# Optimization experiments

Hardware: AMD Instinct MI355X
Metric: run time of the kernel (lower is better)

## Reference

```python
import jax, jax.numpy as jnp
import numpy as np

B, N, D, C, E, K = 8, 8192, 128, 128, 8, 2


def setup_inputs() -> dict:
    key = jax.random.key(0)
    k0, k1, k2 = jax.random.split(key, 3)
    x = jax.random.normal(k0, (B, N, D), dtype=jnp.float32)
    router_w = jax.random.normal(k1, (D, E), dtype=jnp.float32) * 0.05
    router_b = jnp.zeros((E,), dtype=jnp.float32)
    expert_w = jax.random.normal(k2, (E, D, C), dtype=jnp.float32) * (1.0 / np.sqrt(D))
    expert_b = jnp.zeros((E, C), dtype=jnp.float32)
    return {"x": x, "router_w": router_w, "router_b": router_b,
            "expert_w": expert_w, "expert_b": expert_b}


def reference(x, router_w, router_b, expert_w, expert_b):
    # Router: softmax over experts, then top-k gating with renormalization.
    router_probs = jax.nn.softmax(x @ router_w + router_b, axis=-1)      # [B,N,E]
    top_p, top_i = jax.lax.top_k(router_probs, K)                        # [B,N,K]
    top_p = top_p / jnp.sum(top_p, axis=-1, keepdims=True)
    # Naive all-expert dense compute (faithful to original): [B,N,E,C]
    expert_out = jnp.einsum('bnd,edc->bnec', x, expert_w) + expert_b
    # Gather the K selected experts per token: [B,N,K,C]
    gathered = jnp.take_along_axis(expert_out, top_i[..., None], axis=2)
    # Weighted combine over selected experts: [B,N,C]
    return jnp.einsum('bnk,bnkc->bnc', top_p, gathered)
```

## Files before the change

kernel.cpp:

```cpp
#include <hip/hip_runtime.h>
#include <hip/hip_bf16.h>
#include <stdint.h>

#define Dd 128
#define Cc 128
#define Ee 8
#define TM 64
#define NTOK 65536

using f32x4  = __attribute__((ext_vector_type(4))) float;
using short8 = __attribute__((ext_vector_type(8))) short;
typedef unsigned short u16;

__device__ inline u16 f2bf(float f) {
    union { __hip_bfloat16 h; u16 u; } cv;
    cv.h = __float2bfloat16(f);
    return cv.u;
}

__global__ __launch_bounds__(256) void transpose_w(const float* __restrict__ w,
                                                   u16* __restrict__ wt) {
    int idx = blockIdx.x * 256 + threadIdx.x;
    int d = idx & 127;
    int c = (idx >> 7) & 127;
    int e = idx >> 14;
    wt[idx] = f2bf(w[(e << 14) + (d << 7) + c]);
}

__global__ __launch_bounds__(256, 3) void moe_main(
    const float* __restrict__ x,
    const float* __restrict__ rw,
    const float* __restrict__ rb,
    const float* __restrict__ eb,
    const u16*   __restrict__ wt,
    float*       __restrict__ out)
{
    __shared__ __align__(16) unsigned char ldsA[Cc * Dd * 2];
    __shared__ __align__(16) u16 Xs[TM * Dd];
    __shared__ float glg[TM * Ee];

    float* Xf = (float*)ldsA;
    u16*   Ws = (u16*)ldsA;

    const int tid = threadIdx.x;
    const int t0  = blockIdx.x * TM;

    {
        const float4* src = (const float4*)(x + (size_t)t0 * Dd);
        float4* dst = (float4*)Xf;
        #pragma unroll
        for (int j = 0; j < 8; ++j) dst[j * 256 + tid] = src[j * 256 + tid];
    }
    __syncthreads();

    #pragma unroll
    for (int i = 0; i < 2; ++i) {
        int p  = tid * 2 + i;
        int tk = p >> 3, e = p & 7;
        double acc = (double)rb[e];
        const float* xr = Xf + tk * Dd;
        for (int d = 0; d < Dd; ++d)
            acc += (double)xr[d] * (double)rw[d * Ee + e];
        glg[p] = (float)acc;
    }

    #pragma unroll
    for (int j = 0; j < 4; ++j) {
        int fc = j * 256 + tid;
        int r = fc >> 4, c = fc & 15;
        const float4* s = (const float4*)(Xf + r * Dd + c * 8);
        float4 a = s[0], b = s[1];
        short8 v;
        v[0] = (short)f2bf(a.x); v[1] = (short)f2bf(a.y);
        v[2] = (short)f2bf(a.z); v[3] = (short)f2bf(a.w);
        v[4] = (short)f2bf(b.x); v[5] = (short)f2bf(b.y);
        v[6] = (short)f2bf(b.z); v[7] = (short)f2bf(b.w);
        *(short8*)&Xs[r * Dd + (((c ^ (r & 7)) & 15) << 3)] = v;
    }
    __syncthreads();

    if (tid < TM) {
        float l[Ee];
        #pragma unroll
        for (int e = 0; e < Ee; ++e) l[e] = glg[tid * Ee + e];
        int e0 = 0;
        #pragma unroll
        for (int e = 1; e < Ee; ++e) if (l[e] > l[e0]) e0 = e;
        int e1 = (e0 == 0) ? 1 : 0;
        #pragma unroll
        for (int e = 0; e < Ee; ++e)
            if (e != e0 && l[e] > l[e1]) e1 = e;
        float g1 = __expf(l[e1] - l[e0]);
        float s  = 1.0f + g1;
        float g0 = 1.0f / s; g1 = g1 / s;
        #pragma unroll
        for (int e = 0; e < Ee; ++e) glg[tid * Ee + e] = 0.0f;
        glg[tid * Ee + e0] = g0;
        glg[tid * Ee + e1] = g1;
    }

    const int lane = tid & 63;
    const int wv   = tid >> 6;
    const int m0   = (wv >> 1) * 32;
    const int n0   = (wv & 1) * 64;
    const int ln15 = lane & 15;
    const int kg   = lane >> 4;

    f32x4 oacc[2][4] = {};

    for (int e = 0; e < Ee; ++e) {
        __syncthreads();
        {
            const u16* src = wt + ((size_t)e << 14);
            #pragma unroll
            for (int j = 0; j < 8; ++j) {
                int fc = j * 256 + tid;
                int r = fc >> 4, c = fc & 15;
                short8 v = *(const short8*)(src + (fc << 3));
                *(short8*)&Ws[r * Dd + (((c ^ (r & 7)) & 15) << 3)] = v;
            }
        }
        __syncthreads();

        f32x4 acc[2][4] = {};
        #pragma unroll
        for (int ks = 0; ks < 4; ++ks) {
            short8 af[2], bfr[4];
            #pragma unroll
            for (int mi = 0; mi < 2; ++mi) {
                int r = m0 + mi * 16 + ln15;
                af[mi] = *(const short8*)
                    &Xs[r * Dd + ((((ks * 4 + kg) ^ (r & 7)) & 15) << 3)];
            }
            #pragma unroll
            for (int ni = 0; ni < 4; ++ni) {
                int r = n0 + ni * 16 + ln15;
                bfr[ni] = *(const short8*)
                    &Ws[r * Dd + ((((ks * 4 + kg) ^ (r & 7)) & 15) << 3)];
            }
            #pragma unroll
            for (int mi = 0; mi < 2; ++mi)
                #pragma unroll
                for (int ni = 0; ni < 4; ++ni)
                    acc[mi][ni] = __builtin_amdgcn_mfma_f32_16x16x32_bf16(
                        af[mi], bfr[ni], acc[mi][ni], 0, 0, 0);
        }

        #pragma unroll
        for (int mi = 0; mi < 2; ++mi) {
            #pragma unroll
            for (int r = 0; r < 4; ++r) {
                float g = glg[(m0 + mi * 16 + kg * 4 + r) * Ee + e];
                #pragma unroll
                for (int ni = 0; ni < 4; ++ni) {
                    float b = eb[e * Cc + n0 + ni * 16 + ln15];
                    oacc[mi][ni][r] += g * (acc[mi][ni][r] + b);
                }
            }
        }
    }

    #pragma unroll
    for (int mi = 0; mi < 2; ++mi)
        #pragma unroll
        for (int r = 0; r < 4; ++r) {
            size_t row = (size_t)(t0 + m0 + mi * 16 + kg * 4 + r);
            #pragma unroll
            for (int ni = 0; ni < 4; ++ni)
                out[row * Cc + n0 + ni * 16 + ln15] = oacc[mi][ni][r];
        }
}

extern "C" void kernel_launch(void* const* d_in, const int* in_sizes, int n_in,
                              void* d_out, int out_size, void* d_ws, size_t ws_size,
                              hipStream_t stream) {
    const float* x  = (const float*)d_in[0];
    const float* rw = (const float*)d_in[1];
    const float* rb = (const float*)d_in[2];
    const float* ew = (const float*)d_in[3];
    const float* eb = (const float*)d_in[4];
    float* out = (float*)d_out;
    u16* wt = (u16*)d_ws;

    transpose_w<<<dim3(512), dim3(256), 0, stream>>>(ew, wt);
    moe_main<<<dim3(NTOK / TM), dim3(256), 0, stream>>>(x, rw, rb, eb, wt, out);
}
```

Measured before the change: 144.3 us.

## Double-buffer expert weights with async LDS loads and keep activations in registers

Expert weights are now written pre-swizzled by the transpose kernel. The main kernel streams each expert's weights into one of two LDS buffers with global_load_lds, so the next expert's tile loads while the current expert's MFMAs run. Activation fragments are loaded straight from global memory into registers as bf16 instead of going through LDS. The router top-2 selection is deferred until after the first expert's matmul. This removes the per-expert load/sync serialization and the X staging, at the cost of more LDS per block (occupancy bound drops from 3 to 2) and a dependence on async-copy completion being ordered before the barriers.

Result: slower. 179.8 us (+24.6%).

```diff
diff --git a/kernel.cpp b/kernel.cpp
--- a/kernel.cpp
+++ b/kernel.cpp
@@ -24,10 +24,28 @@
     int d = idx & 127;
     int c = (idx >> 7) & 127;
     int e = idx >> 14;
-    wt[idx] = f2bf(w[(e << 14) + (d << 7) + c]);
-}
-
-__global__ __launch_bounds__(256, 3) void moe_main(
+    int slot = (d >> 3) ^ (c & 7);
+    wt[(e << 14) + (c << 7) + (slot << 3) + (d & 7)] =
+        f2bf(w[(e << 14) + (d << 7) + c]);
+}
+
+__device__ __forceinline__ void stage_expert(const u16* __restrict__ wt, int e,
+                                             u16* dst, int tid) {
+    const u16* src = wt + ((size_t)e << 14);
+    int wave = tid >> 6;
+    #pragma unroll
+    for (int j = 0; j < 8; ++j) {
+        int chunk = (j << 8) + tid;
+        const u16* g = src + (chunk << 3);
+        u16* l = dst + ((((j << 8) + (wave << 6))) << 3);
+        __builtin_amdgcn_global_load_lds(
+            (const __attribute__((address_space(1))) unsigned int*)g,
+            (__attribute__((address_space(3))) unsigned int*)l,
+            16, 0, 0);
+    }
+}
+
+__global__ __launch_bounds__(256, 2) void moe_main(
     const float* __restrict__ x,
     const float* __restrict__ rw,
     const float* __restrict__ rb,
@@ -35,128 +53,129 @@
     const u16*   __restrict__ wt,
     float*       __restrict__ out)
 {
-    __shared__ __align__(16) unsigned char ldsA[Cc * Dd * 2];
-    __shared__ __align__(16) u16 Xs[TM * Dd];
+    __shared__ __align__(16) u16 Ws[2][Cc * Dd];
     __shared__ float glg[TM * Ee];
 
-    float* Xf = (float*)ldsA;
-    u16*   Ws = (u16*)ldsA;
-
-    const int tid = threadIdx.x;
-    const int t0  = blockIdx.x * TM;
-
-    {
-        const float4* src = (const float4*)(x + (size_t)t0 * Dd);
-        float4* dst = (float4*)Xf;
-        #pragma unroll
-        for (int j = 0; j < 8; ++j) dst[j * 256 + tid] = src[j * 256 + tid];
-    }
-    __syncthreads();
-
-    #pragma unroll
-    for (int i = 0; i < 2; ++i) {
-        int p  = tid * 2 + i;
-        int tk = p >> 3, e = p & 7;
-        double acc = (double)rb[e];
-        const float* xr = Xf + tk * Dd;
-        for (int d = 0; d < Dd; ++d)
-            acc += (double)xr[d] * (double)rw[d * Ee + e];
-        glg[p] = (float)acc;
-    }
-
-    #pragma unroll
-    for (int j = 0; j < 4; ++j) {
-        int fc = j * 256 + tid;
-        int r = fc >> 4, c = fc & 15;
-        const float4* s = (const float4*)(Xf + r * Dd + c * 8);
-        float4 a = s[0], b = s[1];
-        short8 v;
-        v[0] = (short)f2bf(a.x); v[1] = (short)f2bf(a.y);
-        v[2] = (short)f2bf(a.z); v[3] = (short)f2bf(a.w);
-        v[4] = (short)f2bf(b.x); v[5] = (short)f2bf(b.y);
-        v[6] = (short)f2bf(b.z); v[7] = (short)f2bf(b.w);
-        *(short8*)&Xs[r * Dd + (((c ^ (r & 7)) & 15) << 3)] = v;
-    }
-    __syncthreads();
-
-    if (tid < TM) {
-        float l[Ee];
-        #pragma unroll
-        for (int e = 0; e < Ee; ++e) l[e] = glg[tid * Ee + e];
-        int e0 = 0;
-        #pragma unroll
-        for (int e = 1; e < Ee; ++e) if (l[e] > l[e0]) e0 = e;
-        int e1 = (e0 == 0) ? 1 : 0;
-        #pragma unroll
-        for (int e = 0; e < Ee; ++e)
-            if (e != e0 && l[e] > l[e1]) e1 = e;
-        float g1 = __expf(l[e1] - l[e0]);
-        float s  = 1.0f + g1;
-        float g0 = 1.0f / s; g1 = g1 / s;
-        #pragma unroll
-        for (int e = 0; e < Ee; ++e) glg[tid * Ee + e] = 0.0f;
-        glg[tid * Ee + e0] = g0;
-        glg[tid * Ee + e1] = g1;
-    }
-
+    const int tid  = threadIdx.x;
+    const int t0   = blockIdx.x * TM;
     const int lane = tid & 63;
-    const int wv   = tid >> 6;
-    const int m0   = (wv >> 1) * 32;
-    const int n0   = (wv & 1) * 64;
+    const int wave = tid >> 6;
+    const int m0   = (wave >> 1) * 32;
+    const int n0   = (wave & 1) * 64;
     const int ln15 = lane & 15;
     const int kg   = lane >> 4;
 
+    stage_expert(wt, 0, Ws[0], tid);
+
+    {
+        int p  = tid * 2;
+        int tk = p >> 3, e0 = p & 7;
+        const float4* xr = (const float4*)(x + (size_t)(t0 + tk) * Dd);
+        double a0 = (double)rb[e0], a1 = (double)rb[e0 + 1];
+        #pragma unroll 8
+        for (int q = 0; q < 32; ++q) {
+            float4 v = xr[q];
+            #pragma unroll
+            for (int u = 0; u < 4; ++u) {
+                double xv = (double)((const float*)&v)[u];
+                a0 += xv * (double)rw[(q * 4 + u) * Ee + e0];
+                a1 += xv * (double)rw[(q * 4 + u) * Ee + e0 + 1];
+            }
+        }
+        glg[p] = (float)a0;
+        glg[p + 1] = (float)a1;
+    }
+
+    short8 af[2][4];
+    #pragma unroll
+    for (int mi = 0; mi < 2; ++mi) {
+        int r = t0 + m0 + mi * 16 + ln15;
+        #pragma unroll
+        for (int ks = 0; ks < 4; ++ks) {
+            const float4* s = (const float4*)(x + (size_t)r * Dd + (ks * 4 + kg) * 8);
+            float4 a = s[0], b = s[1];
+            short8 v;
+            v[0] = (short)f2bf(a.x); v[1] = (short)f2bf(a.y);
+            v[2] = (short)f2bf(a.z); v[3] = (short)f2bf(a.w);
+            v[4] = (short)f2bf(b.x); v[5] = (short)f2bf(b.y);
+            v[6] = (short)f2bf(b.z); v[7] = (short)f2bf(b.w);
+            af[mi][ks] = v;
+        }
+    }
+
+    __syncthreads();
+
     f32x4 oacc[2][4] = {};
 
     for (int e = 0; e < Ee; ++e) {
-        __syncthreads();
-        {
-            const u16* src = wt + ((size_t)e << 14);
-            #pragma unroll
-            for (int j = 0; j < 8; ++j) {
-                int fc = j * 256 + tid;
-                int r = fc >> 4, c = fc & 15;
-                short8 v = *(const short8*)(src + (fc << 3));
-                *(short8*)&Ws[r * Dd + (((c ^ (r & 7)) & 15) << 3)] = v;
-            }
-        }
-        __syncthreads();
+        const u16* wsc = Ws[e & 1];
+        if (e < Ee - 1) stage_expert(wt, e + 1, Ws[(e + 1) & 1], tid);
 
         f32x4 acc[2][4] = {};
         #pragma unroll
         for (int ks = 0; ks < 4; ++ks) {
-            short8 af[2], bfr[4];
-            #pragma unroll
-            for (int mi = 0; mi < 2; ++mi) {
-                int r = m0 + mi * 16 + ln15;
-                af[mi] = *(const short8*)
-                    &Xs[r * Dd + ((((ks * 4 + kg) ^ (r & 7)) & 15) << 3)];
-            }
+            short8 bfr[4];
+            int cc = ks * 4 + kg;
             #pragma unroll
             for (int ni = 0; ni < 4; ++ni) {
                 int r = n0 + ni * 16 + ln15;
-                bfr[ni] = *(const short8*)
-                    &Ws[r * Dd + ((((ks * 4 + kg) ^ (r & 7)) & 15) << 3)];
+                bfr[ni] = *(const short8*)&wsc[r * Dd + ((cc ^ (r & 7)) << 3)];
             }
             #pragma unroll
             for (int mi = 0; mi < 2; ++mi)
                 #pragma unroll
                 for (int ni = 0; ni < 4; ++ni)
                     acc[mi][ni] = __builtin_amdgcn_mfma_f32_16x16x32_bf16(
-                        af[mi], bfr[ni], acc[mi][ni], 0, 0, 0);
-        }
-
-        #pragma unroll
-        for (int mi = 0; mi < 2; ++mi) {
-            #pragma unroll
-            for (int r = 0; r < 4; ++r) {
-                float g = glg[(m0 + mi * 16 + kg * 4 + r) * Ee + e];
-                #pragma unroll
-                for (int ni = 0; ni < 4; ++ni) {
-                    float b = eb[e * Cc + n0 + ni * 16 + ln15];
-                    oacc[mi][ni][r] += g * (acc[mi][ni][r] + b);
+                        af[mi][ks], bfr[ni], acc[mi][ni], 0, 0, 0);
+        }
+
+        if (e == 0) {
+            if (tid < TM) {
+                float l[Ee];
+                #pragma unroll
+                for (int k = 0; k < Ee; ++k) l[k] = glg[tid * Ee + k];
+                int e0 = 0;
+                #pragma unroll
+                for (int k = 1; k < Ee; ++k) if (l[k] > l[e0]) e0 = k;
+                int e1 = (e0 == 0) ? 1 : 0;
+                #pragma unroll
+                for (int k = 0; k < Ee; ++k)
+                    if (k != e0 && l[k] > l[e1]) e1 = k;
+                float g1 = __expf(l[e1] - l[e0]);
+                float s  = 1.0f + g1;
+                float g0 = 1.0f / s; g1 = g1 / s;
+                #pragma unroll
+                for (int k = 0; k < Ee; ++k) glg[tid * Ee + k] = 0.0f;
+                glg[tid * Ee + e0] = g0;
+                glg[tid * Ee + e1] = g1;
+            }
+            __syncthreads();
+            float bb[4];
+            #pragma unroll
+            for (int ni = 0; ni < 4; ++ni) bb[ni] = eb[e * Cc + n0 + ni * 16 + ln15];
+            #pragma unroll
+            for (int mi = 0; mi < 2; ++mi)
+                #pragma unroll
+                for (int r = 0; r < 4; ++r) {
+                    float g = glg[(m0 + mi * 16 + kg * 4 + r) * Ee + e];
+                    #pragma unroll
+                    for (int ni = 0; ni < 4; ++ni)
+                        oacc[mi][ni][r] += g * (acc[mi][ni][r] + bb[ni]);
                 }
-            }
+        } else {
+            float bb[4];
+            #pragma unroll
+            for (int ni = 0; ni < 4; ++ni) bb[ni] = eb[e * Cc + n0 + ni * 16 + ln15];
+            #pragma unroll
+            for (int mi = 0; mi < 2; ++mi)
+                #pragma unroll
+                for (int r = 0; r < 4; ++r) {
+                    float g = glg[(m0 + mi * 16 + kg * 4 + r) * Ee + e];
+                    #pragma unroll
+                    for (int ni = 0; ni < 4; ++ni)
+                        oacc[mi][ni][r] += g * (acc[mi][ni][r] + bb[ni]);
+                }
+            __syncthreads();
         }
     }
 
```
